# Performance work log

Measured on AMD Instinct MI355X. Metric: run time of the kernel, lower is better.

The kernel has to match this reference:

```python
import jax, jax.numpy as jnp
import numpy as np

N = 100000
E_ADJ = 800000
E_RAY = 800000
IN_DIM = 2
HID = 64
HEADS = 2
NEG_SLOPE = 0.2  # PyG GATv2Conv default


def setup_inputs() -> dict:
    key = jax.random.key(0)
    ks = jax.random.split(key, 16)
    s = 0.1
    p = lambda k, shape: (jax.random.normal(k, shape, jnp.float32) * s)
    inp = {
        "x": jax.random.normal(ks[0], (N, IN_DIM), jnp.float32),
        "edge_adj": jax.random.randint(ks[1], (2, E_ADJ), 0, N, jnp.int32),
        "edge_ray": jax.random.randint(ks[2], (2, E_RAY), 0, N, jnp.int32),
        # layer 1 params, stacked over the 2 relation types [adjacent, ray]
        "l1_Wl": p(ks[3], (2, IN_DIM, HEADS * HID)),
        "l1_bl": jnp.zeros((2, HEADS * HID), jnp.float32),
        "l1_Wr": p(ks[4], (2, IN_DIM, HEADS * HID)),
        "l1_br": jnp.zeros((2, HEADS * HID), jnp.float32),
        "l1_att": p(ks[5], (2, HEADS, HID)),
        "l1_bias": jnp.zeros((2, HID), jnp.float32),
        # layer 2 params
        "l2_Wl": p(ks[6], (2, HID, HEADS * HID)),
        "l2_bl": jnp.zeros((2, HEADS * HID), jnp.float32),
        "l2_Wr": p(ks[7], (2, HID, HEADS * HID)),
        "l2_br": jnp.zeros((2, HEADS * HID), jnp.float32),
        "l2_att": p(ks[8], (2, HEADS, HID)),
        "l2_bias": jnp.zeros((2, HID), jnp.float32),
    }
    return inp


def _gatv2(x, src, dst, Wl, bl, Wr, br, att, bias):
    # GATv2Conv, concat=False, add_self_loops=False (PyG semantics)
    n = x.shape[0]
    H, C = att.shape
    xl = (x @ Wl + bl).reshape(n, H, C)  # source transform
    xr = (x @ Wr + br).reshape(n, H, C)  # target transform
    e = jax.nn.leaky_relu(xl[src] + xr[dst], NEG_SLOPE)  # [E,H,C]
    score = jnp.einsum('ehc,hc->eh', e, att)             # [E,H]
    # segment softmax over incoming edges per destination (per head)
    m = jax.ops.segment_max(score, dst, num_segments=n)  # only gathered at non-empty segs
    ex = jnp.exp(score - m[dst])
    denom = jax.ops.segment_sum(ex, dst, num_segments=n)
    alpha = ex / (denom[dst] + 1e-16)                    # [E,H]
    out = jax.ops.segment_sum(xl[src] * alpha[:, :, None], dst, num_segments=n)  # [N,H,C]
    return out.mean(axis=1) + bias                       # concat=False -> head mean


def _hetero_layer(x, ea, er, Wl, bl, Wr, br, att, bias):
    o_adj = _gatv2(x, ea[0], ea[1], Wl[0], bl[0], Wr[0], br[0], att[0], bias[0])
    o_ray = _gatv2(x, er[0], er[1], Wl[1], bl[1], Wr[1], br[1], att[1], bias[1])
    return 0.5 * (o_adj + o_ray)  # HeteroConv aggr='mean' over 2 relations


def reference(x, edge_adj, edge_ray,
              l1_Wl, l1_bl, l1_Wr, l1_br, l1_att, l1_bias,
              l2_Wl, l2_bl, l2_Wr, l2_br, l2_att, l2_bias):
    h = _hetero_layer(x, edge_adj, edge_ray, l1_Wl, l1_bl, l1_Wr, l1_br, l1_att, l1_bias)
    h = jax.nn.relu(h)
    out = _hetero_layer(h, edge_adj, edge_ray, l2_Wl, l2_bl, l2_Wr, l2_br, l2_att, l2_bias)
    return out
```

## Files before the change

### kernel.cpp

```cpp
#include <hip/hip_runtime.h>
#include <hip/hip_bf16.h>

typedef __hip_bfloat16 bf16;
typedef unsigned int uint;
typedef unsigned short ushort;
typedef __attribute__((ext_vector_type(8))) short short8;
typedef __attribute__((ext_vector_type(4))) float floatx4;

#define N_NODES 100000
#define N_PAD   100096
#define E_EDGES 800000
#define NBLK    98
#define EBLK    3125
#define RBLK    782

static __device__ __forceinline__ uint packbf(float a, float b) {
  bf16 x = __float2bfloat16(a), y = __float2bfloat16(b);
  ushort ux = *reinterpret_cast<ushort*>(&x);
  ushort uy = *reinterpret_cast<ushort*>(&y);
  return (uint)ux | ((uint)uy << 16);
}
static __device__ __forceinline__ float lo16(uint u) { return __uint_as_float(u << 16); }
static __device__ __forceinline__ float hi16(uint u) { return __uint_as_float(u & 0xffff0000u); }

__global__ __launch_bounds__(256) void rank_k(
    const int* __restrict__ dst0, const int* __restrict__ dst1,
    int* fi0, int* fi1, int* __restrict__ rk0, int* __restrict__ rk1) {
  int base = blockIdx.x * 256 + threadIdx.x;
  int rel = blockIdx.y;
  const int* dst = rel ? dst1 : dst0;
  int* fi = rel ? fi1 : fi0;
  int* rk = rel ? rk1 : rk0;
#pragma unroll
  for (int k = 0; k < 4; ++k) {
    int i = base + k * (RBLK * 256);
    if (i < E_EDGES) {
      int d = dst[i];
      rk[i] = atomicAdd(&fi[d], 1);
    }
  }
}

__global__ __launch_bounds__(256) void scat_rank_k(
    const int* __restrict__ src0, const int* __restrict__ dst0,
    const int* __restrict__ src1, const int* __restrict__ dst1,
    const int* __restrict__ rk0, const int* __restrict__ rk1,
    const int* __restrict__ rp0, const int* __restrict__ rp1,
    int2* __restrict__ csd0, int2* __restrict__ csd1) {
  int i = blockIdx.x * 256 + threadIdx.x;
  int rel = blockIdx.y;
  const int* src = rel ? src1 : src0;
  const int* dst = rel ? dst1 : dst0;
  const int* rk = rel ? rk1 : rk0;
  const int* rp = rel ? rp1 : rp0;
  int2* csd = rel ? csd1 : csd0;
  int d = dst[i];
  int s = src[i];
  int pos = rp[d] + rk[i];
  csd[pos] = make_int2(s, d);
}

__global__ void scan_blk_k(const int* __restrict__ deg0, const int* __restrict__ deg1,
                           int* rp0, int* rp1, int* bsum) {
  __shared__ int s[1024];
  int r = blockIdx.y;
  const int* deg = r ? deg1 : deg0;
  int* rp = r ? rp1 : rp0;
  int i = blockIdx.x * 1024 + threadIdx.x;
  int v = (i < N_NODES) ? deg[i] : 0;
  s[threadIdx.x] = v;
  __syncthreads();
  for (int off = 1; off < 1024; off <<= 1) {
    int t = (threadIdx.x >= off) ? s[threadIdx.x - off] : 0;
    __syncthreads();
    s[threadIdx.x] += t;
    __syncthreads();
  }
  if (i < N_NODES) rp[i] = s[threadIdx.x] - v;
  if (threadIdx.x == 1023) bsum[r * NBLK + blockIdx.x] = s[1023];
}

__global__ void scan_top_k(int* bsum, int* rp0, int* rp1) {
  __shared__ int s[128];
  int r = blockIdx.x;
  int v = (threadIdx.x < NBLK) ? bsum[r * NBLK + threadIdx.x] : 0;
  s[threadIdx.x] = v;
  __syncthreads();
  for (int off = 1; off < 128; off <<= 1) {
    int t = (threadIdx.x >= off) ? s[threadIdx.x - off] : 0;
    __syncthreads();
    s[threadIdx.x] += t;
    __syncthreads();
  }
  if (threadIdx.x < NBLK) bsum[r * NBLK + threadIdx.x] = s[threadIdx.x] - v;
  if (threadIdx.x == 127) (r ? rp1 : rp0)[N_NODES] = s[127];
}

__global__ void scan_add_k(const int* __restrict__ bsum,
                           int* rp0, int* rp1, int* fi0, int* fi1) {
  int r = blockIdx.y;
  int i = blockIdx.x * 1024 + threadIdx.x;
  if (i >= N_NODES) return;
  int* rp = r ? rp1 : rp0;
  int* fi = r ? fi1 : fi0;
  int val = rp[i] + bsum[r * NBLK + blockIdx.x];
  rp[i] = val;
  fi[i] = val;
}

__global__ void wprep_k(const float* __restrict__ Wl, const float* __restrict__ Wr,
                        short* __restrict__ WT,
                        const float* __restrict__ l1Wl, const float* __restrict__ l1bl,
                        const float* __restrict__ l1Wr, const float* __restrict__ l1br,
                        const float* __restrict__ l1att, float* __restrict__ L1C,
                        float* __restrict__ SCG) {
  if (blockIdx.x == 128) {
    int t = threadIdx.x;
    {
      int rel = t >> 7, c = t & 127;
      int ch = c >> 2, o = c & 3;
      float* g = SCG + rel * 768 + ch * 24;
      g[0 + o]  = l1bl[rel * 128 + c] + l1br[rel * 128 + c];
      g[4 + o]  = l1Wr[rel * 256 + c];
      g[8 + o]  = l1Wr[rel * 256 + 128 + c];
      g[12 + o] = l1Wl[rel * 256 + c];
      g[16 + o] = l1Wl[rel * 256 + 128 + c];
      g[20 + o] = l1att[rel * 128 + c];
    }
    if (t < 20) {
      int rel = t / 10, rem = t % 10, h = rem / 5, v = rem % 5;
      const float* a = l1att + rel * 128 + h * 64;
      float sum = 0.f;
      for (int c = 0; c < 64; ++c) {
        int cc = h * 64 + c;
        float val;
        if (v == 0)      val = l1bl[rel * 128 + cc] + l1br[rel * 128 + cc];
        else if (v == 1) val = l1Wr[rel * 256 + cc];
        else if (v == 2) val = l1Wr[rel * 256 + 128 + cc];
        else if (v == 3) val = l1Wl[rel * 256 + cc];
        else             val = l1Wl[rel * 256 + 128 + cc];
        sum += a[c] * val;
      }
      L1C[t] = sum;
    }
    return;
  }
  int id2 = blockIdx.x * 256 + threadIdx.x;
  int rel = id2 >> 14;
  int id = id2 & 16383;
  int c = id >> 6, k = id & 63;
  const float* W = (c < 128) ? (Wl + rel * 8192) : (Wr + rel * 8192);
  int cc = c & 127;
  bf16 b = __float2bfloat16(W[k * 128 + cc]);
  WT[rel * 16384 + c * 64 + k] = *reinterpret_cast<short*>(&b);
}

__global__ __launch_bounds__(256) void l1score_k(
    const int2* __restrict__ csd0, const int2* __restrict__ csd1,
    const float* __restrict__ x,
    const float* __restrict__ scg, const float* __restrict__ l1c,
    float4* __restrict__ EX4) {
  int rel = blockIdx.y;
  const int2* csd = rel ? csd1 : csd0;
  const float* sC = scg + rel * 768;
  const float* C = l1c + rel * 10;
  float q00 = C[0], qv00 = C[1], qv10 = C[2], qw00 = C[3], qw10 = C[4];
  float q01 = C[5], qv01 = C[6], qv11 = C[7], qw01 = C[8], qw11 = C[9];
  int i = blockIdx.x * 256 + threadIdx.x;
  int2 sd = csd[i];
  int s = sd.x, d = sd.y;
  float2 xs = *(const float2*)(x + 2 * s);
  float2 xd = *(const float2*)(x + 2 * d);
  float t0a = 0.f, t0b = 0.f, t1a = 0.f, t1b = 0.f;
#pragma unroll
  for (int ch = 0; ch < 32; ++ch) {
    const float4* cp = (const float4*)(sC + ch * 24);
    float4 bb = cp[0], v0 = cp[1], v1 = cp[2], w0 = cp[3], w1 = cp[4], aa = cp[5];
    float e0 = bb.x + xd.x * v0.x + xd.y * v1.x + xs.x * w0.x + xs.y * w1.x;
    float e1 = bb.y + xd.x * v0.y + xd.y * v1.y + xs.x * w0.y + xs.y * w1.y;
    float e2 = bb.z + xd.x * v0.z + xd.y * v1.z + xs.x * w0.z + xs.y * w1.z;
    float e3 = bb.w + xd.x * v0.w + xd.y * v1.w + xs.x * w0.w + xs.y * w1.w;
    if (ch < 16) {
      t0a = fmaf(aa.x, fabsf(e0), t0a); t0b = fmaf(aa.y, fabsf(e1), t0b);
      t0a = fmaf(aa.z, fabsf(e2), t0a); t0b = fmaf(aa.w, fabsf(e3), t0b);
    } else {
      t1a = fmaf(aa.x, fabsf(e0), t1a); t1b = fmaf(aa.y, fabsf(e1), t1b);
      t1a = fmaf(aa.z, fabsf(e2), t1a); t1b = fmaf(aa.w, fabsf(e3), t1b);
    }
  }
  float T0 = t0a + t0b, T1 = t1a + t1b;
  float lin0 = q00 + xd.x * qv00 + xd.y * qv10 + xs.x * qw00 + xs.y * qw10;
  float lin1 = q01 + xd.x * qv01 + xd.y * qv11 + xs.x * qw01 + xs.y * qw11;
  float p0 = fmaf(0.4f, T0, 0.6f * lin0);
  float p1 = fmaf(0.4f, T1, 0.6f * lin1);
  EX4[(size_t)rel * E_EDGES + i] = make_float4(__expf(p0), __expf(p1), xs.x, xs.y);
}

__global__ __launch_bounds__(256) void l1aggfin_k(
    const int* __restrict__ rp0, const int* __restrict__ rp1,
    const float4* __restrict__ EX4,
    const float* __restrict__ Wl, const float* __restrict__ bl,
    const float* __restrict__ bias, uint2* __restrict__ HB2) {
  __shared__ __align__(16) float sNA[64][12];
  int t = threadIdx.x;
  int g = blockIdx.x * 64 + (t >> 2);
  int k = t & 3;
  float p0 = 0.f, p1 = 0.f, p2 = 0.f, p3 = 0.f, p4 = 0.f, p5 = 0.f;
  float p6 = 0.f, p7 = 0.f, p8 = 0.f, p9 = 0.f, p10 = 0.f, p11 = 0.f;
  if (g < N_NODES) {
    {
      int beg = rp0[g], end = rp0[g + 1];
      for (int j = beg + k; j < end; j += 4) {
        float4 e = EX4[j];
        p0 += e.x; p1 = fmaf(e.x, e.z, p1); p2 = fmaf(e.x, e.w, p2);
        p3 += e.y; p4 = fmaf(e.y, e.z, p4); p5 = fmaf(e.y, e.w, p5);
      }
    }
    {
      const float4* E1 = EX4 + E_EDGES;
      int beg = rp1[g], end = rp1[g + 1];
      for (int j = beg + k; j < end; j += 4) {
        float4 e = E1[j];
        p6 += e.x; p7 = fmaf(e.x, e.z, p7); p8 = fmaf(e.x, e.w, p8);
        p9 += e.y; p10 = fmaf(e.y, e.z, p10); p11 = fmaf(e.y, e.w, p11);
      }
    }
  }
#define RED4(v) v += __shfl_xor(v, 1); v += __shfl_xor(v, 2);
  RED4(p0) RED4(p1) RED4(p2) RED4(p3) RED4(p4) RED4(p5)
  RED4(p6) RED4(p7) RED4(p8) RED4(p9) RED4(p10) RED4(p11)
#undef RED4
  {
    int dl = t >> 2;
    if (k == 0)      *(float4*)(&sNA[dl][0]) = make_float4(p0, p1, p2, p3);
    else if (k == 1) *(float4*)(&sNA[dl][4]) = make_float4(p4, p5, p6, p7);
    else if (k == 2) *(float4*)(&sNA[dl][8]) = make_float4(p8, p9, p10, p11);
  }
  __syncthreads();
#pragma unroll
  for (int rep = 0; rep < 4; ++rep) {
    int idx = rep * 256 + t;
    int dl = idx >> 4, l = idx & 15;
    int d = blockIdx.x * 64 + dl;
    if (d >= N_NODES) continue;
    int c0 = 4 * l;
    const float* na = sNA[dl];
    float out0 = 0.f, out1 = 0.f, out2 = 0.f, out3 = 0.f;
#pragma unroll
    for (int r = 0; r < 2; ++r) {
      float a0c = 0.f, a1c = 0.f, a2c = 0.f, a3c = 0.f;
#pragma unroll
      for (int h = 0; h < 2; ++h) {
        float den = na[r * 6 + h * 3 + 0];
        float A0  = na[r * 6 + h * 3 + 1];
        float A1  = na[r * 6 + h * 3 + 2];
        float inv = 1.f / (den + 1e-16f);
        float a0 = A0 * inv, a1 = A1 * inv, S = den * inv;
        float4 W0 = *(const float4*)(Wl + r * 256 + h * 64 + c0);
        float4 W1 = *(const float4*)(Wl + r * 256 + 128 + h * 64 + c0);
        float4 B  = *(const float4*)(bl + r * 128 + h * 64 + c0);
        a0c += a0 * W0.x + a1 * W1.x + S * B.x;
        a1c += a0 * W0.y + a1 * W1.y + S * B.y;
        a2c += a0 * W0.z + a1 * W1.z + S * B.z;
        a3c += a0 * W0.w + a1 * W1.w + S * B.w;
      }
      float4 bi = *(const float4*)(bias + r * 64 + c0);
      out0 += 0.5f * a0c + bi.x;
      out1 += 0.5f * a1c + bi.y;
      out2 += 0.5f * a2c + bi.z;
      out3 += 0.5f * a3c + bi.w;
    }
    out0 = fmaxf(0.5f * out0, 0.f); out1 = fmaxf(0.5f * out1, 0.f);
    out2 = fmaxf(0.5f * out2, 0.f); out3 = fmaxf(0.5f * out3, 0.f);
    HB2[(size_t)d * 16 + l] = make_uint2(packbf(out0, out1), packbf(out2, out3));
  }
}

__global__ __launch_bounds__(256) void mfma_t_k(const bf16* __restrict__ HB,
                                                const short* __restrict__ WTb,
                                                const float* __restrict__ blb,
                                                const float* __restrict__ brb,
                                                bf16* __restrict__ XL0,
                                                bf16* __restrict__ XR0,
                                                bf16* __restrict__ XL1,
                                                bf16* __restrict__ XR1) {
  __shared__ short sW[256 * 72];
  int rel = blockIdx.z;
  const short* WT = WTb + rel * 16384;
  const float* bl = blb + rel * 128;
  const float* br = brb + rel * 128;
  bf16* XLp = rel ? XL1 : XL0;
  bf16* XRp = rel ? XR1 : XR0;
  int t = threadIdx.x;
#pragma unroll
  for (int i = 0; i < 8; ++i) {
    int chunk = t + i * 256;
    int c = chunk >> 3, off = (chunk & 7) * 8;
    *(short8*)(&sW[c * 72 + off]) = *(const short8*)(WT + chunk * 8);
  }
  __syncthreads();
  int wave = t >> 6, lane = t & 63;
  int q = lane >> 4, m = lane & 15;
  int rowbase = blockIdx.x * 128 + wave * 32;
  short8 afr[2][2];
#pragma unroll
  for (int rt = 0; rt < 2; ++rt)
#pragma unroll
    for (int kh = 0; kh < 2; ++kh) {
      size_t row = (size_t)(rowbase + rt * 16 + m);
      afr[rt][kh] = *(const short8*)((const short*)HB + row * 64 + kh * 32 + q * 8);
    }
  for (int ct = 0; ct < 16; ++ct) {
    int col = ct * 16 + m;
    short8 b0 = *(const short8*)(&sW[col * 72 + q * 8]);
    short8 b1 = *(const short8*)(&sW[col * 72 + 32 + q * 8]);
    int c0 = ct * 16 + q * 4;
    int c128 = c0 & 127;
    const float* bp = (ct < 8) ? bl : br;
    bf16* X = (ct < 8) ? XLp : XRp;
    float4 bv = *(const float4*)(bp + c128);
#pragma unroll
    for (int rt = 0; rt < 2; ++rt) {
      floatx4 acc = {0.f, 0.f, 0.f, 0.f};
      acc = __builtin_amdgcn_mfma_f32_16x16x32_bf16(b0, afr[rt][0], acc, 0, 0, 0);
      acc = __builtin_amdgcn_mfma_f32_16x16x32_bf16(b1, afr[rt][1], acc, 0, 0, 0);
      int node = rowbase + rt * 16 + m;
      if (node < N_NODES) {
        uint u0 = packbf(acc[0] + bv.x, acc[1] + bv.y);
        uint u1 = packbf(acc[2] + bv.z, acc[3] + bv.w);
        *(uint2*)((ushort*)X + (size_t)node * 128 + c128) = make_uint2(u0, u1);
      }
    }
  }
}

struct EdgeAcc { float a0, a1, a2, a3, den; };

static __device__ __forceinline__ void edge_step(
    uint2 u, float xr0, float xr1, float xr2, float xr3,
    float at0, float at1, float at2, float at3, EdgeAcc& A) {
  float x0 = lo16(u.x), x1 = hi16(u.x), x2 = lo16(u.y), x3 = hi16(u.y);
  float e0 = x0 + xr0; e0 = fmaxf(e0, 0.2f * e0);
  float e1 = x1 + xr1; e1 = fmaxf(e1, 0.2f * e1);
  float e2 = x2 + xr2; e2 = fmaxf(e2, 0.2f * e2);
  float e3 = x3 + xr3; e3 = fmaxf(e3, 0.2f * e3);
  float p = e0 * at0 + e1 * at1 + e2 * at2 + e3 * at3;
  p += __shfl_xor(p, 1);
  p += __shfl_xor(p, 2);
  p += __shfl_xor(p, 4);
  p += __shfl_xor(p, 8);
  float ex = __expf(p);
  A.den += ex;
  A.a0 += ex * x0; A.a1 += ex * x1; A.a2 += ex * x2; A.a3 += ex * x3;
}

__global__ __launch_bounds__(256) void aggf_k(
    const int* __restrict__ rp0, const int2* __restrict__ csd0,
    const int* __restrict__ rp1, const int2* __restrict__ csd1,
    const bf16* __restrict__ XL0, const bf16* __restrict__ XR0,
    const bf16* __restrict__ XL1, const bf16* __restrict__ XR1,
    const float* __restrict__ att,
    const float* __restrict__ bias,
    float* __restrict__ outf) {
  int d = (blockIdx.x * 256 + threadIdx.x) >> 6;
  int lane = threadIdx.x & 63;
  if (d >= N_NODES) return;
  int half = lane >> 5;
  int l = lane & 31;
  int beg0 = rp0[d], end0 = rp0[d + 1];
  int beg1 = rp1[d], end1 = rp1[d + 1];
  const float* at = att + 4 * l;
  const float* bt = att + 128 + 4 * l;
  float at0 = at[0], at1 = at[1], at2 = at[2], at3 = at[3];
  float bt0 = bt[0], bt1 = bt[1], bt2 = bt[2], bt3 = bt[3];
  uint2 ur0 = *(const uint2*)(XR0 + (size_t)d * 128 + 4 * l);
  uint2 ur1 = *(const uint2*)(XR1 + (size_t)d * 128 + 4 * l);
  float xa0 = lo16(ur0.x), xa1 = hi16(ur0.x), xa2 = lo16(ur0.y), xa3 = hi16(ur0.y);
  float xb0 = lo16(ur1.x), xb1 = hi16(ur1.x), xb2 = lo16(ur1.y), xb3 = hi16(ur1.y);
  EdgeAcc A = {0.f, 0.f, 0.f, 0.f, 0.f};
  EdgeAcc B = {0.f, 0.f, 0.f, 0.f, 0.f};
  {
    int j = beg0 + half;
    for (; j + 2 < end0; j += 4) {
      int sA = csd0[j].x, sB = csd0[j + 2].x;
      uint2 uA = *(const uint2*)(XL0 + (size_t)sA * 128 + 4 * l);
      uint2 uB = *(const uint2*)(XL0 + (size_t)sB * 128 + 4 * l);
      edge_step(uA, xa0, xa1, xa2, xa3, at0, at1, at2, at3, A);
      edge_step(uB, xa0, xa1, xa2, xa3, at0, at1, at2, at3, A);
    }
    for (; j < end0; j += 2) {
      int s = csd0[j].x;
      uint2 u = *(const uint2*)(XL0 + (size_t)s * 128 + 4 * l);
      edge_step(u, xa0, xa1, xa2, xa3, at0, at1, at2, at3, A);
    }
  }
  {
    int j = beg1 + half;
    for (; j + 2 < end1; j += 4) {
      int sA = csd1[j].x, sB = csd1[j + 2].x;
      uint2 uA = *(const uint2*)(XL1 + (size_t)sA * 128 + 4 * l);
      uint2 uB = *(const uint2*)(XL1 + (size_t)sB * 128 + 4 * l);
      edge_step(uA, xb0, xb1, xb2, xb3, bt0, bt1, bt2, bt3, B);
      edge_step(uB, xb0, xb1, xb2, xb3, bt0, bt1, bt2, bt3, B);
    }
    for (; j < end1; j += 2) {
      int s = csd1[j].x;
      uint2 u = *(const uint2*)(XL1 + (size_t)s * 128 + 4 * l);
      edge_step(u, xb0, xb1, xb2, xb3, bt0, bt1, bt2, bt3, B);
    }
  }
#define C32(v) v += __shfl_xor(v, 32);
  C32(A.den) C32(A.a0) C32(A.a1) C32(A.a2) C32(A.a3)
  C32(B.den) C32(B.a0) C32(B.a1) C32(B.a2) C32(B.a3)
#undef C32
  float invA = 1.f / (A.den + 1e-16f);
  float invB = 1.f / (B.den + 1e-16f);
  A.a0 *= invA; A.a1 *= invA; A.a2 *= invA; A.a3 *= invA;
  B.a0 *= invB; B.a1 *= invB; B.a2 *= invB; B.a3 *= invB;
  float t0 = 0.5f * (A.a0 + __shfl_xor(A.a0, 16));
  float t1 = 0.5f * (A.a1 + __shfl_xor(A.a1, 16));
  float t2 = 0.5f * (A.a2 + __shfl_xor(A.a2, 16));
  float t3 = 0.5f * (A.a3 + __shfl_xor(A.a3, 16));
  float u0 = 0.5f * (B.a0 + __shfl_xor(B.a0, 16));
  float u1 = 0.5f * (B.a1 + __shfl_xor(B.a1, 16));
  float u2 = 0.5f * (B.a2 + __shfl_xor(B.a2, 16));
  float u3 = 0.5f * (B.a3 + __shfl_xor(B.a3, 16));
  if (lane >= 16) return;
  int c0 = 4 * lane;
  t0 += bias[c0]; t1 += bias[c0 + 1]; t2 += bias[c0 + 2]; t3 += bias[c0 + 3];
  u0 += bias[64 + c0]; u1 += bias[64 + c0 + 1];
  u2 += bias[64 + c0 + 2]; u3 += bias[64 + c0 + 3];
  float v0 = 0.5f * (t0 + u0);
  float v1 = 0.5f * (t1 + u1);
  float v2 = 0.5f * (t2 + u2);
  float v3 = 0.5f * (t3 + u3);
  *(float4*)(outf + (size_t)d * 64 + c0) = make_float4(v0, v1, v2, v3);
}

extern "C" void kernel_launch(void* const* d_in, const int* in_sizes, int n_in,
                              void* d_out, int out_size, void* d_ws, size_t ws_size,
                              hipStream_t stream) {
  const float* x       = (const float*)d_in[0];
  const int*   e_adj   = (const int*)d_in[1];
  const int*   e_ray   = (const int*)d_in[2];
  const float* l1_Wl   = (const float*)d_in[3];
  const float* l1_bl   = (const float*)d_in[4];
  const float* l1_Wr   = (const float*)d_in[5];
  const float* l1_br   = (const float*)d_in[6];
  const float* l1_att  = (const float*)d_in[7];
  const float* l1_bias = (const float*)d_in[8];
  const float* l2_Wl   = (const float*)d_in[9];
  const float* l2_bl   = (const float*)d_in[10];
  const float* l2_Wr   = (const float*)d_in[11];
  const float* l2_br   = (const float*)d_in[12];
  const float* l2_att  = (const float*)d_in[13];
  const float* l2_bias = (const float*)d_in[14];
  float* out = (float*)d_out;

  char* w = (char*)d_ws;
  size_t off = 0;
  auto alloc = [&](size_t bytes) -> char* {
    char* p = w + off;
    off += (bytes + 255) & ~(size_t)255;
    return p;
  };
  bf16* XL0  = (bf16*)alloc((size_t)N_PAD * 128 * 2);
  bf16* XR0  = (bf16*)alloc((size_t)N_PAD * 128 * 2);
  bf16* XL1  = (bf16*)alloc((size_t)N_PAD * 128 * 2);
  bf16* XR1  = (bf16*)alloc((size_t)N_PAD * 128 * 2);
  bf16* HB   = (bf16*)alloc((size_t)N_PAD * 64 * 2);
  short* WT  = (short*)alloc(2 * 16384 * 2);
  int* RP0   = (int*)alloc((size_t)(N_NODES + 1) * 4);
  int* RP1   = (int*)alloc((size_t)(N_NODES + 1) * 4);
  int* FI0   = (int*)alloc((size_t)N_NODES * 4);
  int* FI1   = (int*)alloc((size_t)N_NODES * 4);
  int2* CSD0 = (int2*)alloc((size_t)E_EDGES * 8);
  int2* CSD1 = (int2*)alloc((size_t)E_EDGES * 8);
  int* BSUM  = (int*)alloc(2 * NBLK * 4);
  float* L1C = (float*)alloc(20 * 4);
  float* SCG = (float*)alloc(2 * 768 * 4);

  float4* EX4 = (float4*)XL0;
  int* RK0    = (int*)XL1;
  int* RK1    = (int*)((char*)XL1 + 3200000);

  const int* src_adj = e_adj;
  const int* dst_adj = e_adj + E_EDGES;
  const int* src_ray = e_ray;
  const int* dst_ray = e_ray + E_EDGES;

  const int WNB = (N_NODES * 64) / 256;
  const int MB  = N_PAD / 128;

  size_t fispan = (size_t)((char*)FI1 - (char*)FI0) + (size_t)N_NODES * 4;
  hipMemsetAsync(FI0, 0, fispan, stream);
  rank_k<<<dim3(RBLK, 2), 256, 0, stream>>>(dst_adj, dst_ray, FI0, FI1, RK0, RK1);
  scan_blk_k<<<dim3(NBLK, 2), 1024, 0, stream>>>(FI0, FI1, RP0, RP1, BSUM);
  scan_top_k<<<2, 128, 0, stream>>>(BSUM, RP0, RP1);
  scan_add_k<<<dim3(NBLK, 2), 1024, 0, stream>>>(BSUM, RP0, RP1, FI0, FI1);
  scat_rank_k<<<dim3(EBLK, 2), 256, 0, stream>>>(src_adj, dst_adj, src_ray, dst_ray,
                                                 RK0, RK1, RP0, RP1, CSD0, CSD1);
  wprep_k<<<129, 256, 0, stream>>>(l2_Wl, l2_Wr, WT,
                                   l1_Wl, l1_bl, l1_Wr, l1_br, l1_att, L1C, SCG);

  l1score_k<<<dim3(EBLK, 2), 256, 0, stream>>>(CSD0, CSD1, x, SCG, L1C, EX4);
  l1aggfin_k<<<(N_NODES + 63) / 64, 256, 0, stream>>>(RP0, RP1, EX4,
                                                      l1_Wl, l1_bl, l1_bias,
                                                      (uint2*)HB);

  mfma_t_k<<<dim3(MB, 1, 2), 256, 0, stream>>>(HB, WT, l2_bl, l2_br,
                                               XL0, XR0, XL1, XR1);
  aggf_k<<<WNB, 256, 0, stream>>>(RP0, CSD0, RP1, CSD1, XL0, XR0, XL1, XR1,
                                  l2_att, l2_bias, out);
}
```

Before: 411.1 us.

## Software-pipeline edge gathers and simplify GATv2 score with DPP reductions

The per-edge gather loop becomes a software pipeline that prefetches source indices and XL rows several edges ahead. The loads for both relations are issued up front so memory latency overlaps with compute. The leaky-ReLU score is rewritten algebraically as 0.6*x + 0.4*|x|. This splits out the destination-only term, which is computed once per node as a per-destination constant. The 16-lane shuffle reduction is replaced with DPP row-shift adds. Together these cut ALU work and cross-lane latency per edge, but they add register pressure and extra clamped loads.

After: 412.8 us. No clear change (+0.4%).

```diff
diff --git a/kernel.cpp b/kernel.cpp
--- a/kernel.cpp
+++ b/kernel.cpp
@@ -22,6 +22,18 @@
 }
 static __device__ __forceinline__ float lo16(uint u) { return __uint_as_float(u << 16); }
 static __device__ __forceinline__ float hi16(uint u) { return __uint_as_float(u & 0xffff0000u); }
+
+static __device__ __forceinline__ float rsum16(float p) {
+  p += __int_as_float(__builtin_amdgcn_update_dpp(
+      0, __float_as_int(p), 0x128, 0xF, 0xF, false));
+  p += __int_as_float(__builtin_amdgcn_update_dpp(
+      0, __float_as_int(p), 0x124, 0xF, 0xF, false));
+  p += __int_as_float(__builtin_amdgcn_update_dpp(
+      0, __float_as_int(p), 0x122, 0xF, 0xF, false));
+  p += __int_as_float(__builtin_amdgcn_update_dpp(
+      0, __float_as_int(p), 0x121, 0xF, 0xF, false));
+  return p;
+}
 
 __global__ __launch_bounds__(256) void rank_k(
     const int* __restrict__ dst0, const int* __restrict__ dst1,
@@ -338,20 +350,25 @@
 
 static __device__ __forceinline__ void edge_step(
     uint2 u, float xr0, float xr1, float xr2, float xr3,
-    float at0, float at1, float at2, float at3, EdgeAcc& A) {
+    float at0, float at1, float at2, float at3, float q06, EdgeAcc& A) {
   float x0 = lo16(u.x), x1 = hi16(u.x), x2 = lo16(u.y), x3 = hi16(u.y);
-  float e0 = x0 + xr0; e0 = fmaxf(e0, 0.2f * e0);
-  float e1 = x1 + xr1; e1 = fmaxf(e1, 0.2f * e1);
-  float e2 = x2 + xr2; e2 = fmaxf(e2, 0.2f * e2);
-  float e3 = x3 + xr3; e3 = fmaxf(e3, 0.2f * e3);
-  float p = e0 * at0 + e1 * at1 + e2 * at2 + e3 * at3;
-  p += __shfl_xor(p, 1);
-  p += __shfl_xor(p, 2);
-  p += __shfl_xor(p, 4);
-  p += __shfl_xor(p, 8);
-  float ex = __expf(p);
+  float e0 = x0 + xr0, e1 = x1 + xr1, e2 = x2 + xr2, e3 = x3 + xr3;
+  float sa = at0 * fabsf(e0);
+  sa = fmaf(at1, fabsf(e1), sa);
+  sa = fmaf(at2, fabsf(e2), sa);
+  sa = fmaf(at3, fabsf(e3), sa);
+  float sx = at0 * x0;
+  sx = fmaf(at1, x1, sx);
+  sx = fmaf(at2, x2, sx);
+  sx = fmaf(at3, x3, sx);
+  float p = fmaf(0.6f, sx, 0.4f * sa);
+  p = rsum16(p);
+  float ex = __expf(p + q06);
   A.den += ex;
-  A.a0 += ex * x0; A.a1 += ex * x1; A.a2 += ex * x2; A.a3 += ex * x3;
+  A.a0 = fmaf(ex, x0, A.a0);
+  A.a1 = fmaf(ex, x1, A.a1);
+  A.a2 = fmaf(ex, x2, A.a2);
+  A.a3 = fmaf(ex, x3, A.a3);
 }
 
 __global__ __launch_bounds__(256) void aggf_k(
@@ -377,37 +394,45 @@
   uint2 ur1 = *(const uint2*)(XR1 + (size_t)d * 128 + 4 * l);
   float xa0 = lo16(ur0.x), xa1 = hi16(ur0.x), xa2 = lo16(ur0.y), xa3 = hi16(ur0.y);
   float xb0 = lo16(ur1.x), xb1 = hi16(ur1.x), xb2 = lo16(ur1.y), xb3 = hi16(ur1.y);
+  float qa = at0 * xa0; qa = fmaf(at1, xa1, qa);
+  qa = fmaf(at2, xa2, qa); qa = fmaf(at3, xa3, qa);
+  qa = 0.6f * rsum16(qa);
+  float qb = bt0 * xb0; qb = fmaf(bt1, xb1, qb);
+  qb = fmaf(bt2, xb2, qb); qb = fmaf(bt3, xb3, qb);
+  qb = 0.6f * rsum16(qb);
   EdgeAcc A = {0.f, 0.f, 0.f, 0.f, 0.f};
   EdgeAcc B = {0.f, 0.f, 0.f, 0.f, 0.f};
-  {
-    int j = beg0 + half;
-    for (; j + 2 < end0; j += 4) {
-      int sA = csd0[j].x, sB = csd0[j + 2].x;
-      uint2 uA = *(const uint2*)(XL0 + (size_t)sA * 128 + 4 * l);
-      uint2 uB = *(const uint2*)(XL0 + (size_t)sB * 128 + 4 * l);
-      edge_step(uA, xa0, xa1, xa2, xa3, at0, at1, at2, at3, A);
-      edge_step(uB, xa0, xa1, xa2, xa3, at0, at1, at2, at3, A);
-    }
-    for (; j < end0; j += 2) {
-      int s = csd0[j].x;
-      uint2 u = *(const uint2*)(XL0 + (size_t)s * 128 + 4 * l);
-      edge_step(u, xa0, xa1, xa2, xa3, at0, at1, at2, at3, A);
-    }
-  }
-  {
-    int j = beg1 + half;
-    for (; j + 2 < end1; j += 4) {
-      int sA = csd1[j].x, sB = csd1[j + 2].x;
-      uint2 uA = *(const uint2*)(XL1 + (size_t)sA * 128 + 4 * l);
-      uint2 uB = *(const uint2*)(XL1 + (size_t)sB * 128 + 4 * l);
-      edge_step(uA, xb0, xb1, xb2, xb3, bt0, bt1, bt2, bt3, B);
-      edge_step(uB, xb0, xb1, xb2, xb3, bt0, bt1, bt2, bt3, B);
-    }
-    for (; j < end1; j += 2) {
-      int s = csd1[j].x;
-      uint2 u = *(const uint2*)(XL1 + (size_t)s * 128 + 4 * l);
-      edge_step(u, xb0, xb1, xb2, xb3, bt0, bt1, bt2, bt3, B);
-    }
+  int aj = beg0 + half;
+  int acnt = end0 - aj; acnt = (acnt > 0) ? ((acnt + 1) >> 1) : 0;
+  int alast = (end0 > beg0) ? (end0 - 1) : 0;
+  int ai0 = aj < alast ? aj : alast;
+  int ai1 = aj + 2 < alast ? aj + 2 : alast;
+  int ai2 = aj + 4 < alast ? aj + 4 : alast;
+  int bj = beg1 + half;
+  int bcnt = end1 - bj; bcnt = (bcnt > 0) ? ((bcnt + 1) >> 1) : 0;
+  int blast = (end1 > beg1) ? (end1 - 1) : 0;
+  int bi0 = bj < blast ? bj : blast;
+  int bi1 = bj + 2 < blast ? bj + 2 : blast;
+  int bi2 = bj + 4 < blast ? bj + 4 : blast;
+  int as0 = csd0[ai0].x, as1 = csd0[ai1].x, as2 = csd0[ai2].x;
+  int bs0 = csd1[bi0].x, bs1 = csd1[bi1].x, bs2 = csd1[bi2].x;
+  uint2 au0 = *(const uint2*)(XL0 + (size_t)as0 * 128 + 4 * l);
+  uint2 au1 = *(const uint2*)(XL0 + (size_t)as1 * 128 + 4 * l);
+  uint2 bu0 = *(const uint2*)(XL1 + (size_t)bs0 * 128 + 4 * l);
+  uint2 bu1 = *(const uint2*)(XL1 + (size_t)bs1 * 128 + 4 * l);
+  for (int it = 0; it < acnt; ++it) {
+    uint2 au2 = *(const uint2*)(XL0 + (size_t)as2 * 128 + 4 * l);
+    int jn = aj + 2 * it + 6; jn = jn < alast ? jn : alast;
+    int as3 = csd0[jn].x;
+    edge_step(au0, xa0, xa1, xa2, xa3, at0, at1, at2, at3, qa, A);
+    au0 = au1; au1 = au2; as2 = as3;
+  }
+  for (int it = 0; it < bcnt; ++it) {
+    uint2 bu2 = *(const uint2*)(XL1 + (size_t)bs2 * 128 + 4 * l);
+    int jn = bj + 2 * it + 6; jn = jn < blast ? jn : blast;
+    int bs3 = csd1[jn].x;
+    edge_step(bu0, xb0, xb1, xb2, xb3, bt0, bt1, bt2, bt3, qb, B);
+    bu0 = bu1; bu1 = bu2; bs2 = bs3;
   }
 #define C32(v) v += __shfl_xor(v, 32);
   C32(A.den) C32(A.a0) C32(A.a1) C32(A.a2) C32(A.a3)
```
